# Kernel optimization log

Hardware: AMD Instinct MI355X
Metric: run time of the kernel (lower is better)

## Reference

```python
import jax, jax.numpy as jnp
import numpy as np
from jax import lax

N = 2048        # nodes
F_IN = 512      # input features
D_MODEL = 256
D_INNER = 256   # must equal d_model (shapes in original forward)
DT_RANK = 16
N_STATE = 16    # block ssm state size
LAYER_NUM = 8   # GCN propagation depth == ssm seq len
NUM_CLASSES = 40
HDIM = 8; NHEADS = D_MODEL // HDIM; D_ST2 = 8; D_CONV = 4   # Mamba2 branch
CONV_DIM = D_INNER + 2 * D_ST2
ALPHA = 0.1; GW = 0.5
BN_EPS = 1e-5; RMS_EPS = 1e-5

def setup_inputs():
    key = jax.random.key(0)
    ks = jax.random.split(key, 16)
    def uni(k, shape, s):
        return jax.random.uniform(k, shape, minval=-s, maxval=s, dtype=jnp.float32)
    d_in_proj = 2 * D_INNER + 2 * D_ST2 + NHEADS
    blk_A = jnp.tile(jnp.arange(1, N_STATE + 1, dtype=jnp.float32)[None, :], (D_INNER, 1))
    return {
        "x": jax.random.normal(ks[0], (N, F_IN), dtype=jnp.float32),
        "adj": jax.random.normal(ks[1], (N, N), dtype=jnp.float32) * (0.5 / np.sqrt(N)),
        "lin1_W": uni(ks[2], (F_IN, D_MODEL), 1.0 / np.sqrt(D_MODEL)),
        "m2_in_proj": uni(ks[3], (D_MODEL, d_in_proj), 1.0 / np.sqrt(D_MODEL)),
        "m2_conv_w": uni(ks[4], (CONV_DIM, D_CONV), 1.0 / np.sqrt(D_CONV)),
        "m2_conv_b": jnp.zeros((CONV_DIM,), jnp.float32),
        "m2_dt_bias": uni(ks[5], (NHEADS,), 0.1),
        "m2_A_log": jnp.log(jnp.arange(1, NHEADS + 1, dtype=jnp.float32)),
        "m2_D": jnp.ones((NHEADS,), jnp.float32),
        "m2_norm_w": jnp.ones((D_INNER,), jnp.float32),
        "m2_out_proj": uni(ks[6], (D_INNER, D_MODEL), 1.0 / np.sqrt(D_MODEL)),
        "blk_xproj_W": uni(ks[7], (D_INNER, DT_RANK + 2 * N_STATE), 1.0 / np.sqrt(DT_RANK + 2 * N_STATE)),
        "blk_dtproj_W": uni(ks[8], (DT_RANK, D_INNER), 1.0 / np.sqrt(D_INNER)),
        "blk_A_log": jnp.log(blk_A),
        "blk_D": jnp.ones((D_INNER,), jnp.float32),
        "blk_outproj_W": uni(ks[9], (D_INNER, D_MODEL), 1.0 / np.sqrt(D_MODEL)),
        "bn1_g": jnp.ones((D_MODEL,), jnp.float32),
        "bn1_b": jnp.zeros((D_MODEL,), jnp.float32),
        "bn2_g": jnp.ones((D_MODEL,), jnp.float32),
        "bn2_b": jnp.zeros((D_MODEL,), jnp.float32),
        "lin2_W": uni(ks[10], (D_MODEL, NUM_CLASSES), 1.0 / np.sqrt(NUM_CLASSES)),
    }

def _bn_eval(x, g, b):
    # eval-mode BatchNorm1d with fresh running stats (mean=0, var=1)
    return x * (g / np.sqrt(1.0 + BN_EPS)) + b

def _mamba2(u, in_proj, conv_w, conv_b, dt_bias, A_log, Dp, norm_w, out_proj):
    # u: (b, l, d_model). Mamba2 with expand=1, ngroups=1, headdim=8, d_state=8.
    b, l, _ = u.shape
    zxbcdt = u @ in_proj
    z = zxbcdt[..., :D_INNER]
    xBC = zxbcdt[..., D_INNER:D_INNER + CONV_DIM]
    dt = jax.nn.softplus(zxbcdt[..., -NHEADS:] + dt_bias)          # (b,l,h)
    # causal depthwise conv over sequence
    conv = lax.conv_general_dilated(
        xBC.transpose(0, 2, 1), conv_w[:, None, :], (1,), [(D_CONV - 1, 0)],
        feature_group_count=CONV_DIM)
    xBC = jax.nn.silu(conv.transpose(0, 2, 1) + conv_b)
    xh = xBC[..., :D_INNER].reshape(b, l, NHEADS, HDIM)
    Bm = xBC[..., D_INNER:D_INNER + D_ST2]                          # (b,l,n)
    Cm = xBC[..., D_INNER + D_ST2:]                                 # (b,l,n)
    A = -jnp.exp(A_log)                                             # (h,)
    dA = jnp.exp(dt * A)                                            # (b,l,h)
    dBx = jnp.einsum('blh,bln,blhp->blhpn', dt, Bm, xh)
    def step(s, inp):
        dA_t, dBx_t, C_t = inp
        s = dA_t[:, :, None, None] * s + dBx_t                      # (b,h,p,n)
        return s, jnp.einsum('bhpn,bn->bhp', s, C_t)
    s0 = jnp.zeros((b, NHEADS, HDIM, D_ST2), u.dtype)
    _, ys = lax.scan(step, s0, (dA.transpose(1, 0, 2),
                                dBx.transpose(1, 0, 2, 3, 4),
                                Cm.transpose(1, 0, 2)))
    y = ys.transpose(1, 0, 2, 3) + xh * Dp[None, None, :, None]
    y = y.reshape(b, l, D_INNER)
    g = y * jax.nn.silu(z)                                          # gated RMSNorm
    g = g * lax.rsqrt(jnp.mean(g * g, -1, keepdims=True) + RMS_EPS) * norm_w
    return g @ out_proj

def _gcn_mamba_block(xb, adj, xproj_W, dtproj_W, A_log, Dp, outproj_W):
    # GCN propagation builds the 'sequence' over layers; Mamba selective scan over it.
    feats = [xb]
    xi = xb
    for _ in range(LAYER_NUM - 1):
        xi = adj @ xi
        xi = 0.95 * xi + 0.05 * xb     # alpha=0.05 hardcoded in original forward
        feats.append(xi)
    xs = jnp.stack(feats, axis=1)                                   # (N, L, d)
    x_dbl = jax.nn.relu(xs @ xproj_W)
    delta = jax.nn.softplus(x_dbl[..., :DT_RANK] @ dtproj_W)        # (N,L,d)
    Bm = x_dbl[..., DT_RANK:DT_RANK + N_STATE]
    Cm = x_dbl[..., DT_RANK + N_STATE:]
    A = -jnp.exp(A_log)                                             # (d,n)
    dA = jnp.exp(jnp.einsum('bld,dn->bldn', delta, A))
    dBu = jnp.einsum('bld,bln,bld->bldn', delta, Bm, xs)
    def step(s, inp):
        dA_t, dBu_t, C_t = inp
        s = dA_t * s + dBu_t                                        # (N,d,n)
        return s, jnp.einsum('bdn,bn->bd', s, C_t)
    s0 = jnp.zeros((xs.shape[0], D_INNER, N_STATE), xs.dtype)
    _, ys = lax.scan(step, s0, (dA.transpose(1, 0, 2, 3),
                                dBu.transpose(1, 0, 2, 3),
                                Cm.transpose(1, 0, 2)))
    y = ys.transpose(1, 0, 2) + xs * Dp
    return y @ outproj_W                                            # (N,L,d_model)

def reference(x, adj, lin1_W, m2_in_proj, m2_conv_w, m2_conv_b, m2_dt_bias,
              m2_A_log, m2_D, m2_norm_w, m2_out_proj, blk_xproj_W, blk_dtproj_W,
              blk_A_log, blk_D, blk_outproj_W, bn1_g, bn1_b, bn2_g, bn2_b, lin2_W):
    x_input = x @ lin1_W                                            # (N,d)
    g_in = x_input[None]                                            # (1,N,d)
    m2 = lambda t: _mamba2(t, m2_in_proj, m2_conv_w, m2_conv_b, m2_dt_bias,
                           m2_A_log, m2_D, m2_norm_w, m2_out_proj)
    g_out = m2(g_in) + jnp.flip(m2(jnp.flip(g_in, 1)), 1)
    g_out = jax.nn.relu(g_out)[0] * (1.0 - ALPHA) + ALPHA * x_input
    xb = jax.nn.relu(_bn_eval(x_input, bn1_g, bn1_b))
    all_out = _gcn_mamba_block(xb, adj, blk_xproj_W, blk_dtproj_W,
                               blk_A_log, blk_D, blk_outproj_W)
    output = (all_out[:, -1, :] + x_input) * GW + g_out * (1.0 - GW)
    output = jax.nn.relu(_bn_eval(output, bn2_g, bn2_b))
    all_out = jax.nn.relu(all_out)
    y = output @ lin2_W
    return (all_out, jax.nn.log_softmax(y, axis=-1))
```

## Files before the change

kernel.cpp:

```cpp
#include <hip/hip_runtime.h>
#include <math.h>


typedef _Float16 half8 __attribute__((ext_vector_type(8)));
typedef _Float16 half4v __attribute__((ext_vector_type(4)));
typedef float f32x4 __attribute__((ext_vector_type(4)));

__device__ __forceinline__ float softplus_fast(float x) {
    return fmaxf(x, 0.f) + __logf(1.f + __expf(-fabsf(x)));
}
__device__ __forceinline__ float silu_fast(float x) {
    return __fdividef(x, 1.f + __expf(-x));
}

template<int EPI>
__global__ __launch_bounds__(256) void mm16(
    const _Float16* __restrict__ A16, int lda,
    const _Float16* __restrict__ BT16, int ldb,
    float* __restrict__ dst, _Float16* __restrict__ dst16,
    const _Float16* __restrict__ aux16, _Float16* __restrict__ aux2_16,
    int N, int ldc, int kchunk)
{
    __shared__ _Float16 As[128][40];
    __shared__ _Float16 Bs[64][40];
    const int tid = threadIdx.x;
    const int col0 = blockIdx.x * 64;
    const int row0 = blockIdx.y * 128;
    const int kz = blockIdx.z;
    const int k0 = kz * kchunk;
    const int wave = tid >> 6, lane = tid & 63;
    f32x4 acc[2][4];
    #pragma unroll
    for (int i = 0; i < 2; ++i)
        #pragma unroll
        for (int j = 0; j < 4; ++j)
            acc[i][j] = (f32x4){0.f, 0.f, 0.f, 0.f};
    const int ar = tid >> 1, ac = (tid & 1) * 16;
    const int br = tid >> 2, bc = (tid & 3) * 8;
    const int lrow = lane & 15, kof = (lane >> 4) * 8;
    for (int ks = 0; ks < kchunk; ks += 32) {
        {
            const _Float16* src = A16 + (size_t)(row0 + ar) * lda + k0 + ks + ac;
            *reinterpret_cast<float4*>(&As[ar][ac])     = *reinterpret_cast<const float4*>(src);
            *reinterpret_cast<float4*>(&As[ar][ac + 8]) = *reinterpret_cast<const float4*>(src + 8);
        }
        {
            const _Float16* src = BT16 + (size_t)(col0 + br) * ldb + k0 + ks + bc;
            *reinterpret_cast<float4*>(&Bs[br][bc]) = *reinterpret_cast<const float4*>(src);
        }
        __syncthreads();
        half8 a[2], b[4];
        #pragma unroll
        for (int fr = 0; fr < 2; ++fr)
            a[fr] = *reinterpret_cast<const half8*>(&As[wave * 32 + fr * 16 + lrow][kof]);
        #pragma unroll
        for (int fc = 0; fc < 4; ++fc)
            b[fc] = *reinterpret_cast<const half8*>(&Bs[fc * 16 + lrow][kof]);
        #pragma unroll
        for (int fr = 0; fr < 2; ++fr)
            #pragma unroll
            for (int fc = 0; fc < 4; ++fc)
                acc[fr][fc] = __builtin_amdgcn_mfma_f32_16x16x32_f16(a[fr], b[fc], acc[fr][fc], 0, 0, 0);
        __syncthreads();
    }
    const int col = lane & 15, rbase = (lane >> 4) * 4;
    #pragma unroll
    for (int fr = 0; fr < 2; ++fr)
        #pragma unroll
        for (int fc = 0; fc < 4; ++fc) {
            int c = col0 + fc * 16 + col;
            #pragma unroll
            for (int i = 0; i < 4; ++i) {
                int m = row0 + wave * 32 + fr * 16 + rbase + i;
                float v = acc[fr][fc][i];
                if (EPI == 0) {
                    _Float16* P = dst16 + (size_t)kz * gridDim.y * 128 * 256;
                    P[(size_t)m * 256 + c] = (_Float16)v;
                } else if (EPI == 1) {
                    if (c < N) dst[(size_t)m * ldc + c] = fmaxf(v, 0.f);
                } else if (EPI == 2) {
                    dst16[(size_t)m * 256 + c] =
                        (_Float16)(fmaxf(v, 0.f) * 0.9f + 0.1f * (float)aux16[(size_t)m * 256 + c]);
                } else if (EPI == 3) {
                    int bb = m & 2047, ll = m >> 11;
                    dst[(size_t)((bb << 3) + ll) * 256 + c] = fmaxf(v, 0.f);
                    if (ll == 7) aux2_16[(size_t)bb * 256 + c] = (_Float16)v;
                } else if (EPI == 4) {
                    dst16[(size_t)m * 256 + c] = (_Float16)v;
                } else {
                    if (c < N) dst16[(size_t)m * ldc + c] = (_Float16)v;
                }
            }
        }
}

__global__ __launch_bounds__(256) void k_combine16(
    const _Float16* __restrict__ psum16, const _Float16* __restrict__ xb16,
    _Float16* __restrict__ xi16, _Float16* __restrict__ fT16)
{
    int m0 = (blockIdx.x >> 3) * 32, n0 = (blockIdx.x & 7) * 32;
    int row = threadIdx.x >> 3;
    int c4  = (threadIdx.x & 7) * 4;
    __shared__ float T[32][33];
    size_t idx = (size_t)(m0 + row) * 256 + n0 + c4;
    float s[4] = {0.f, 0.f, 0.f, 0.f};
    #pragma unroll
    for (int q = 0; q < 4; ++q) {
        half4v pv = *reinterpret_cast<const half4v*>(&psum16[idx + (size_t)q * 524288]);
        s[0] += (float)pv[0]; s[1] += (float)pv[1];
        s[2] += (float)pv[2]; s[3] += (float)pv[3];
    }
    half4v xv = *reinterpret_cast<const half4v*>(&xb16[idx]);
    half4v ov;
    #pragma unroll
    for (int j = 0; j < 4; ++j) {
        float v = 0.95f * s[j] + 0.05f * (float)xv[j];
        ov[j] = (_Float16)v;
        T[row][c4 + j] = v;
    }
    *reinterpret_cast<half4v*>(&xi16[idx]) = ov;
    __syncthreads();
    int tx = threadIdx.x & 31, tg = threadIdx.x >> 5;
    #pragma unroll
    for (int j = 0; j < 4; ++j) {
        int n = tg * 4 + j;
        fT16[(size_t)(n0 + n) * 2048 + m0 + tx] = (_Float16)T[tx][n];
    }
}

__global__ __launch_bounds__(256) void k_prep(
    const float* __restrict__ x, const float* __restrict__ adj,
    const float* __restrict__ lin1W, const float* __restrict__ inproj,
    const float* __restrict__ outprj, const float* __restrict__ xprojW,
    const float* __restrict__ boutW,
    _Float16* __restrict__ x16, _Float16* __restrict__ adj16,
    _Float16* __restrict__ lin1WT, _Float16* __restrict__ inprojT,
    _Float16* __restrict__ outprjT, _Float16* __restrict__ xprojT,
    _Float16* __restrict__ WT16)
{
    int b = blockIdx.x, tid = threadIdx.x;
    if (b < 5120) {
        const float* src = (b < 1024) ? x : adj;
        _Float16* o = (b < 1024) ? x16 : adj16;
        int lb = (b < 1024) ? b : b - 1024;
        int i = (lb * 256 + tid) * 4;
        float4 v = *reinterpret_cast<const float4*>(&src[i]);
        half4v h;
        h[0] = (_Float16)v.x; h[1] = (_Float16)v.y; h[2] = (_Float16)v.z; h[3] = (_Float16)v.w;
        *reinterpret_cast<half4v*>(&o[i]) = h;
    } else if (b < 5632) {
        int idx = (b - 5120) * 256 + tid;
        int n = idx >> 9, k = idx & 511;
        lin1WT[idx] = (_Float16)lin1W[(size_t)k * 256 + n];
    } else if (b < 6208) {
        int idx = (b - 5632) * 256 + tid;
        int n = idx >> 8, k = idx & 255;
        inprojT[idx] = (n < 560) ? (_Float16)inproj[(size_t)k * 560 + n] : (_Float16)0.f;
    } else if (b < 6464) {
        int idx = (b - 6208) * 256 + tid;
        int n = idx >> 8, k = idx & 255;
        outprjT[idx] = (_Float16)outprj[(size_t)k * 256 + n];
    } else if (b < 6528) {
        int idx = (b - 6464) * 256 + tid;
        int n = idx >> 8, k = idx & 255;
        xprojT[idx] = (n < 48) ? (_Float16)xprojW[(size_t)k * 48 + n] : (_Float16)0.f;
    } else {
        int idx = (b - 6528) * 256 + tid;
        int n = idx >> 8, k = idx & 255;
        WT16[idx] = (_Float16)boutW[(size_t)k * 256 + n];
    }
}

__global__ __launch_bounds__(256) void k_xb_t16(
    const _Float16* __restrict__ X16, const float* __restrict__ g, const float* __restrict__ b,
    _Float16* __restrict__ f16a, _Float16* __restrict__ fT16)
{
    const float sc = 0.99999500003749951f;
    int m0 = (blockIdx.x >> 3) * 32, n0 = (blockIdx.x & 7) * 32;
    int tx = threadIdx.x & 31, tg = threadIdx.x >> 5;
    __shared__ float T[32][33];
    float gd = g[n0 + tx] * sc, bd = b[n0 + tx];
    #pragma unroll
    for (int i = 0; i < 4; ++i) {
        int m = tg * 4 + i;
        size_t idx = (size_t)(m0 + m) * 256 + n0 + tx;
        float v = fmaxf((float)X16[idx] * gd + bd, 0.f);
        f16a[idx] = (_Float16)v;
        T[m][tx] = v;
    }
    __syncthreads();
    #pragma unroll
    for (int j = 0; j < 4; ++j) {
        int n = tg * 4 + j;
        fT16[(size_t)(n0 + n) * 2048 + m0 + tx] = (_Float16)T[tx][n];
    }
}

__global__ __launch_bounds__(320) void k_conv(
    const _Float16* __restrict__ Z16, const float* __restrict__ w, const float* __restrict__ bconv,
    float* __restrict__ xhf, float* __restrict__ Bf, float* __restrict__ Cf,
    float* __restrict__ xhr, float* __restrict__ Br, float* __restrict__ Cr)
{
    int bx = blockIdx.x;
    int dir = bx >> 11, t = bx & 2047;
    int c = threadIdx.x;
    if (c >= 272) return;
    float acc = bconv[c];
    #pragma unroll
    for (int k = 0; k < 4; ++k) {
        int tt = dir ? (t + 3 - k) : (t - 3 + k);
        if (tt >= 0 && tt < 2048) acc = fmaf(w[c * 4 + k], (float)Z16[(size_t)tt * 560 + 256 + c], acc);
    }
    float v = silu_fast(acc);
    float* xh = dir ? xhr : xhf;
    float* B  = dir ? Br  : Bf;
    float* C  = dir ? Cr  : Cf;
    if (c < 256)       xh[(size_t)t * 256 + c] = v;
    else if (c < 264)  B[(size_t)t * 8 + (c - 256)] = v;
    else               C[(size_t)t * 8 + (c - 264)] = v;
}

__global__ __launch_bounds__(64) void k_scan_m2_p1(
    const _Float16* __restrict__ Z16, const float* __restrict__ dtbias, const float* __restrict__ A_log,
    const float* __restrict__ xhf, const float* __restrict__ Bf, const float* __restrict__ Cf,
    const float* __restrict__ xhr, const float* __restrict__ Br, const float* __restrict__ Cr,
    const float* __restrict__ Dvec,
    float* __restrict__ yf, float* __restrict__ yr,
    float* __restrict__ Ptbuf,
    float* __restrict__ Acbuf,
    float* __restrict__ Sloc)
{
    int bid = blockIdx.x;
    int c  = bid & 31;
    int hh = bid >> 5;
    int dir = hh >> 5, h = hh & 31;
    const float* xhp = dir ? xhr : xhf;
    const float* Bp  = dir ? Br  : Bf;
    const float* Cp  = dir ? Cr  : Cf;
    float* yp        = dir ? yr  : yf;
    int lane = threadIdx.x;
    int p = lane >> 3, n = lane & 7;
    float Dh = Dvec[h];
    __shared__ float dts[64];
    __shared__ float dAs[64];
    __shared__ float Ps[64][8];
    __shared__ float Bs[64][8];
    __shared__ float Cs[64][8];
    __shared__ float Ys[64][8];
    __shared__ float Pts[64];
    const int j0 = c * 64;
    {
        int j = j0 + lane;
        int t = dir ? (2047 - j) : j;
        float v = (float)Z16[(size_t)t * 560 + 528 + h] + dtbias[h];
        float dtv = softplus_fast(v);
        dts[lane] = dtv;
        dAs[lane] = __expf(-dtv * __expf(A_log[h]));
    }
    __syncthreads();
    #pragma unroll
    for (int q = 0; q < 8; ++q) {
        int idx = q * 64 + lane;
        int i = idx >> 3, e = idx & 7;
        int j = j0 + i;
        int t = dir ? (2047 - j) : j;
        Ps[i][e] = dts[i] * xhp[(size_t)t * 256 + h * 8 + e];
        Bs[i][e] = Bp[(size_t)t * 8 + e];
        Cs[i][e] = Cp[(size_t)t * 8 + e];
    }
    __syncthreads();
    float s = 0.f;
    float P = 1.f;
    for (int i = 0; i < 64; ++i) {
        float a = dAs[i];
        float u = Ps[i][p] * Bs[i][n];
        s = fmaf(a, s, u);
        P *= a;
        float yv = s * Cs[i][n];
        yv += __shfl_xor(yv, 1);
        yv += __shfl_xor(yv, 2);
        yv += __shfl_xor(yv, 4);
        if (n == 0) Ys[i][p] = yv;
        if (lane == 0) Pts[i] = P;
    }
    __syncthreads();
    #pragma unroll
    for (int q = 0; q < 8; ++q) {
        int idx = q * 64 + lane;
        int i = idx >> 3, e = idx & 7;
        int j = j0 + i;
        int t = dir ? (2047 - j) : j;
        yp[(size_t)t * 256 + h * 8 + e] = Ys[i][e] + xhp[(size_t)t * 256 + h * 8 + e] * Dh;
    }
    {
        int j = j0 + lane;
        Ptbuf[((size_t)dir * 2048 + j) * 32 + h] = Pts[lane];
    }
    if (lane == 0) Acbuf[hh * 32 + c] = P;
    Sloc[((size_t)hh * 32 + c) * 64 + lane] = s;
}

__global__ __launch_bounds__(64) void k_scan_m2_p2(
    const float* __restrict__ Acbuf, const float* __restrict__ Sloc,
    float* __restrict__ Sstart)
{
    int hh = blockIdx.x;
    int lane = threadIdx.x;
    float s = 0.f;
    for (int c = 0; c < 32; ++c) {
        Sstart[((size_t)hh * 32 + c) * 64 + lane] = s;
        float a = Acbuf[hh * 32 + c];
        s = fmaf(a, s, Sloc[((size_t)hh * 32 + c) * 64 + lane]);
    }
}

__global__ __launch_bounds__(256) void k_gate(
    const _Float16* __restrict__ Z16, const float* __restrict__ yf, const float* __restrict__ yr,
    const float* __restrict__ Cf, const float* __restrict__ Cr,
    const float* __restrict__ Ptbuf, const float* __restrict__ Sstart,
    const float* __restrict__ nw, _Float16* __restrict__ gsum16)
{
    int t = blockIdx.x, d = threadIdx.x;
    int h = d >> 3, p = d & 7;
    __shared__ float Csh[2][8];
    if (d < 8)       Csh[0][d] = Cf[(size_t)t * 8 + d];
    else if (d < 16) Csh[1][d - 8] = Cr[(size_t)t * 8 + (d - 8)];
    __syncthreads();
    int jf = t, jr = 2047 - t;
    int cf = jf >> 6, cr = jr >> 6;
    float Ptf = Ptbuf[((size_t)jf) * 32 + h];
    float Ptr = Ptbuf[((size_t)2048 + jr) * 32 + h];
    const float* ssf = &Sstart[(((size_t)h) * 32 + cf) * 64 + p * 8];
    const float* ssr = &Sstart[(((size_t)(32 + h)) * 32 + cr) * 64 + p * 8];
    float dotf = 0.f, dotr = 0.f;
    #pragma unroll
    for (int n2 = 0; n2 < 8; ++n2) {
        dotf = fmaf(ssf[n2], Csh[0][n2], dotf);
        dotr = fmaf(ssr[n2], Csh[1][n2], dotr);
    }
    float yfv = yf[(size_t)t * 256 + d] + Ptf * dotf;
    float yrv = yr[(size_t)t * 256 + d] + Ptr * dotr;
    float zv = (float)Z16[(size_t)t * 560 + d];
    float sz = silu_fast(zv);
    float gf = yfv * sz;
    float gr = yrv * sz;
    float vf = gf * gf, vr = gr * gr;
    for (int o = 32; o > 0; o >>= 1) { vf += __shfl_down(vf, o); vr += __shfl_down(vr, o); }
    __shared__ float sfa[4], sra[4];
    __shared__ float tot[2];
    int wid = d >> 6;
    if ((d & 63) == 0) { sfa[wid] = vf; sra[wid] = vr; }
    __syncthreads();
    if (d == 0) {
        tot[0] = sfa[0] + sfa[1] + sfa[2] + sfa[3];
        tot[1] = sra[0] + sra[1] + sra[2] + sra[3];
    }
    __syncthreads();
    float inf_ = rsqrtf(tot[0] / 256.f + 1e-5f);
    float inr_ = rsqrtf(tot[1] / 256.f + 1e-5f);
    gsum16[(size_t)t * 256 + d] = (_Float16)((gf * inf_ + gr * inr_) * nw[d]);
}

__global__ __launch_bounds__(256) void k_scan_gcn(
    const float* __restrict__ xdbl,
    const float* __restrict__ dtW,
    const float* __restrict__ A_log,
    const float* __restrict__ Dv,
    _Float16* __restrict__ f16io)
{
    int b = blockIdx.x, d = threadIdx.x;
    __shared__ float xrow[8][48];
    for (int j = d; j < 384; j += 256) {
        int l = j / 48, k = j % 48;
        xrow[l][k] = xdbl[(size_t)(l * 2048 + b) * 48 + k];
    }
    __syncthreads();
    float a[16];
    #pragma unroll
    for (int n = 0; n < 16; ++n) a[n] = -__expf(A_log[d * 16 + n]);
    float Dd = Dv[d];
    float s[16];
    #pragma unroll
    for (int n = 0; n < 16; ++n) s[n] = 0.f;
    for (int l = 0; l < 8; ++l) {
        float accd = 0.f;
        #pragma unroll
        for (int k = 0; k < 16; ++k) accd = fmaf(xrow[l][k], dtW[k * 256 + d], accd);
        float dl = softplus_fast(accd);
        size_t r = (size_t)(l * 2048 + b) * 256 + d;
        float xv = (float)f16io[r];
        float du = dl * xv;
        float y = 0.f;
        #pragma unroll
        for (int n = 0; n < 16; ++n) {
            float dAn = __expf(dl * a[n]);
            s[n] = fmaf(dAn, s[n], du * xrow[l][16 + n]);
            y = fmaf(s[n], xrow[l][32 + n], y);
        }
        f16io[r] = (_Float16)(y + xv * Dd);
    }
}

__global__ __launch_bounds__(256) void k_head(
    const _Float16* __restrict__ lastl16, const _Float16* __restrict__ X16,
    const _Float16* __restrict__ gout16,
    const float* __restrict__ g2, const float* __restrict__ b2, const float* __restrict__ W2,
    float* __restrict__ out1)
{
    int b = blockIdx.x, d = threadIdx.x;
    __shared__ float ov[256];
    __shared__ float yv[40];
    const float sc = 0.99999500003749951f;
    float v = ((float)lastl16[(size_t)b * 256 + d] + (float)X16[(size_t)b * 256 + d]) * 0.5f
              + (float)gout16[(size_t)b * 256 + d] * 0.5f;
    v = v * (g2[d] * sc) + b2[d];
    ov[d] = fmaxf(v, 0.f);
    __syncthreads();
    if (d < 40) {
        float acc = 0.f;
        for (int k = 0; k < 256; ++k) acc = fmaf(ov[k], W2[k * 40 + d], acc);
        yv[d] = acc;
    }
    __syncthreads();
    if (d < 40) {
        float m = -1e30f;
        for (int j = 0; j < 40; ++j) m = fmaxf(m, yv[j]);
        float se = 0.f;
        for (int j = 0; j < 40; ++j) se += expf(yv[j] - m);
        out1[(size_t)b * 40 + d] = yv[d] - m - logf(se);
    }
}

extern "C" void kernel_launch(void* const* d_in, const int* in_sizes, int n_in,
                              void* d_out, int out_size, void* d_ws, size_t ws_size,
                              hipStream_t stream)
{
    const float* x      = (const float*)d_in[0];
    const float* adj    = (const float*)d_in[1];
    const float* lin1W  = (const float*)d_in[2];
    const float* inproj = (const float*)d_in[3];
    const float* convw  = (const float*)d_in[4];
    const float* convb  = (const float*)d_in[5];
    const float* dtbias = (const float*)d_in[6];
    const float* m2Alog = (const float*)d_in[7];
    const float* m2D    = (const float*)d_in[8];
    const float* normw  = (const float*)d_in[9];
    const float* outprj = (const float*)d_in[10];
    const float* xprojW = (const float*)d_in[11];
    const float* dtprjW = (const float*)d_in[12];
    const float* bAlog  = (const float*)d_in[13];
    const float* bD     = (const float*)d_in[14];
    const float* boutW  = (const float*)d_in[15];
    const float* bn1g   = (const float*)d_in[16];
    const float* bn1b   = (const float*)d_in[17];
    const float* bn2g   = (const float*)d_in[18];
    const float* bn2b   = (const float*)d_in[19];
    const float* lin2W  = (const float*)d_in[20];
    float* out = (float*)d_out;
    float* ws  = (float*)d_ws;

    float* xhf   = ws + 1802240;
    float* Bf    = ws + 2326528;
    float* Cf    = ws + 2342912;
    float* xhr   = ws + 2359296;
    float* Br    = ws + 2883584;
    float* Cr    = ws + 2899968;
    float* yf    = ws + 2916352;
    float* yr    = ws + 3440640;
    float* xdbl  = ws + 9207808;
    float* scr    = ws + 10518528;
    float* Ptbuf  = scr;
    float* Acbuf  = scr + 131072;
    float* Sloc   = scr + 133120;
    float* Sstart = scr + 264192;
    _Float16* psum16 = (_Float16*)(ws + 10518528);
    _Float16* Z16       = (_Float16*)(ws + 524288);
    _Float16* gout16    = (_Float16*)(ws + 4489216);
    _Float16* lastl16   = (_Float16*)(ws + 9994240);
    _Float16* adj16h    = (_Float16*)(ws + 14712832);
    _Float16* fT16A     = (_Float16*)(ws + 16809984);
    _Float16* WT16h     = (_Float16*)(ws + 17072128);
    _Float16* x16       = (_Float16*)(ws + 17104896);
    _Float16* lin1WT16  = (_Float16*)(ws + 17629184);
    _Float16* inprojT16 = (_Float16*)(ws + 17694720);
    _Float16* outprjT16 = (_Float16*)(ws + 17768448);
    _Float16* xprojT16  = (_Float16*)(ws + 17801216);
    _Float16* X16       = (_Float16*)(ws + 17809408);
    _Float16* gsum16    = (_Float16*)(ws + 18071552);
    _Float16* feats16a  = (_Float16*)(ws + 18333696);
    (void)ws_size; (void)in_sizes; (void)n_in; (void)out_size;

    dim3 blk(256);
    k_prep<<<dim3(6784), blk, 0, stream>>>(x, adj, lin1W, inproj, outprj, xprojW, boutW,
                                           x16, adj16h, lin1WT16, inprojT16, outprjT16,
                                           xprojT16, WT16h);
    mm16<4><<<dim3(4, 16, 1), blk, 0, stream>>>(x16, 512, lin1WT16, 512, nullptr, X16, nullptr, nullptr, 256, 256, 512);
    mm16<5><<<dim3(9, 16, 1), blk, 0, stream>>>(X16, 256, inprojT16, 256, nullptr, Z16, nullptr, nullptr, 560, 560, 256);
    k_conv<<<dim3(4096), dim3(320), 0, stream>>>(Z16, convw, convb, xhf, Bf, Cf, xhr, Br, Cr);
    k_scan_m2_p1<<<dim3(2048), dim3(64), 0, stream>>>(Z16, dtbias, m2Alog, xhf, Bf, Cf, xhr, Br, Cr,
                                                      m2D, yf, yr, Ptbuf, Acbuf, Sloc);
    k_scan_m2_p2<<<dim3(64), dim3(64), 0, stream>>>(Acbuf, Sloc, Sstart);
    k_gate<<<dim3(2048), blk, 0, stream>>>(Z16, yf, yr, Cf, Cr, Ptbuf, Sstart, normw, gsum16);
    mm16<2><<<dim3(4, 16, 1), blk, 0, stream>>>(gsum16, 256, outprjT16, 256, nullptr, gout16, X16, nullptr, 256, 256, 256);
    k_xb_t16<<<dim3(512), blk, 0, stream>>>(X16, bn1g, bn1b, feats16a, fT16A);
    for (int i = 1; i < 8; ++i) {
        mm16<0><<<dim3(4, 16, 4), blk, 0, stream>>>(adj16h, 2048, fT16A, 2048, nullptr, psum16, nullptr, nullptr, 256, 256, 512);
        k_combine16<<<dim3(512), blk, 0, stream>>>(psum16, feats16a,
                                                   feats16a + (size_t)i * 524288, fT16A);
    }
    mm16<1><<<dim3(1, 128, 1), blk, 0, stream>>>(feats16a, 256, xprojT16, 256, xdbl, nullptr, nullptr, nullptr, 48, 48, 256);
    k_scan_gcn<<<dim3(2048), blk, 0, stream>>>(xdbl, dtprjW, bAlog, bD, feats16a);
    mm16<3><<<dim3(4, 128, 1), blk, 0, stream>>>(feats16a, 256, WT16h, 256, out, nullptr, nullptr, lastl16, 256, 256, 256);
    k_head<<<dim3(2048), blk, 0, stream>>>(lastl16, X16, gout16, bn2g, bn2b, lin2W, out + 4194304);
}
```

Before: 240.1 us.

## Fuse depthwise conv into scan/gate kernels and double split-K for adjacency matmul

Removes the separate k_conv kernel and its fp32 intermediate buffers (xh, B, C for both directions); the conv+SiLU is recomputed on the fly inside the scan kernel and the gate kernel, which now read Z16 directly. The per-layer adjacency GEMM goes from 4 to 8 split-K chunks of 256, and the combine kernel sums 8 partials, raising block count for the small 2048x256 output. Tradeoffs: redundant conv work (B/C recomputed per head block), more partial-sum traffic, and the loops are no longer unrolled.

Result: no change. 243.9 us (+1.6%).

```diff
diff --git a/kernel.cpp b/kernel.cpp
--- a/kernel.cpp
+++ b/kernel.cpp
@@ -11,6 +11,19 @@
 }
 __device__ __forceinline__ float silu_fast(float x) {
     return __fdividef(x, 1.f + __expf(-x));
+}
+__device__ __forceinline__ float conv_silu(
+    const _Float16* __restrict__ Z16, const float* __restrict__ w,
+    const float* __restrict__ b, int ch, int t, int dir)
+{
+    float acc = b[ch];
+    #pragma unroll
+    for (int k = 0; k < 4; ++k) {
+        int tt = dir ? (t + 3 - k) : (t - 3 + k);
+        if (tt >= 0 && tt < 2048)
+            acc = fmaf(w[ch * 4 + k], (float)Z16[(size_t)tt * 560 + 256 + ch], acc);
+    }
+    return silu_fast(acc);
 }
 
 template<int EPI>
@@ -105,7 +118,7 @@
     size_t idx = (size_t)(m0 + row) * 256 + n0 + c4;
     float s[4] = {0.f, 0.f, 0.f, 0.f};
     #pragma unroll
-    for (int q = 0; q < 4; ++q) {
+    for (int q = 0; q < 8; ++q) {
         half4v pv = *reinterpret_cast<const half4v*>(&psum16[idx + (size_t)q * 524288]);
         s[0] += (float)pv[0]; s[1] += (float)pv[1];
         s[2] += (float)pv[2]; s[3] += (float)pv[3];
@@ -196,34 +209,9 @@
     }
 }
 
-__global__ __launch_bounds__(320) void k_conv(
-    const _Float16* __restrict__ Z16, const float* __restrict__ w, const float* __restrict__ bconv,
-    float* __restrict__ xhf, float* __restrict__ Bf, float* __restrict__ Cf,
-    float* __restrict__ xhr, float* __restrict__ Br, float* __restrict__ Cr)
-{
-    int bx = blockIdx.x;
-    int dir = bx >> 11, t = bx & 2047;
-    int c = threadIdx.x;
-    if (c >= 272) return;
-    float acc = bconv[c];
-    #pragma unroll
-    for (int k = 0; k < 4; ++k) {
-        int tt = dir ? (t + 3 - k) : (t - 3 + k);
-        if (tt >= 0 && tt < 2048) acc = fmaf(w[c * 4 + k], (float)Z16[(size_t)tt * 560 + 256 + c], acc);
-    }
-    float v = silu_fast(acc);
-    float* xh = dir ? xhr : xhf;
-    float* B  = dir ? Br  : Bf;
-    float* C  = dir ? Cr  : Cf;
-    if (c < 256)       xh[(size_t)t * 256 + c] = v;
-    else if (c < 264)  B[(size_t)t * 8 + (c - 256)] = v;
-    else               C[(size_t)t * 8 + (c - 264)] = v;
-}
-
 __global__ __launch_bounds__(64) void k_scan_m2_p1(
     const _Float16* __restrict__ Z16, const float* __restrict__ dtbias, const float* __restrict__ A_log,
-    const float* __restrict__ xhf, const float* __restrict__ Bf, const float* __restrict__ Cf,
-    const float* __restrict__ xhr, const float* __restrict__ Br, const float* __restrict__ Cr,
+    const float* __restrict__ convw, const float* __restrict__ convb,
     const float* __restrict__ Dvec,
     float* __restrict__ yf, float* __restrict__ yr,
     float* __restrict__ Ptbuf,
@@ -234,15 +222,13 @@
     int c  = bid & 31;
     int hh = bid >> 5;
     int dir = hh >> 5, h = hh & 31;
-    const float* xhp = dir ? xhr : xhf;
-    const float* Bp  = dir ? Br  : Bf;
-    const float* Cp  = dir ? Cr  : Cf;
-    float* yp        = dir ? yr  : yf;
+    float* yp = dir ? yr : yf;
     int lane = threadIdx.x;
     int p = lane >> 3, n = lane & 7;
     float Dh = Dvec[h];
     __shared__ float dts[64];
     __shared__ float dAs[64];
+    __shared__ float xhs[64][8];
     __shared__ float Ps[64][8];
     __shared__ float Bs[64][8];
     __shared__ float Cs[64][8];
@@ -258,15 +244,16 @@
         dAs[lane] = __expf(-dtv * __expf(A_log[h]));
     }
     __syncthreads();
-    #pragma unroll
     for (int q = 0; q < 8; ++q) {
         int idx = q * 64 + lane;
         int i = idx >> 3, e = idx & 7;
         int j = j0 + i;
         int t = dir ? (2047 - j) : j;
-        Ps[i][e] = dts[i] * xhp[(size_t)t * 256 + h * 8 + e];
-        Bs[i][e] = Bp[(size_t)t * 8 + e];
-        Cs[i][e] = Cp[(size_t)t * 8 + e];
+        float xh = conv_silu(Z16, convw, convb, h * 8 + e, t, dir);
+        xhs[i][e] = xh;
+        Ps[i][e] = dts[i] * xh;
+        Bs[i][e] = conv_silu(Z16, convw, convb, 256 + e, t, dir);
+        Cs[i][e] = conv_silu(Z16, convw, convb, 264 + e, t, dir);
     }
     __syncthreads();
     float s = 0.f;
@@ -284,13 +271,12 @@
         if (lane == 0) Pts[i] = P;
     }
     __syncthreads();
-    #pragma unroll
     for (int q = 0; q < 8; ++q) {
         int idx = q * 64 + lane;
         int i = idx >> 3, e = idx & 7;
         int j = j0 + i;
         int t = dir ? (2047 - j) : j;
-        yp[(size_t)t * 256 + h * 8 + e] = Ys[i][e] + xhp[(size_t)t * 256 + h * 8 + e] * Dh;
+        yp[(size_t)t * 256 + h * 8 + e] = Ys[i][e] + xhs[i][e] * Dh;
     }
     {
         int j = j0 + lane;
@@ -316,15 +302,15 @@
 
 __global__ __launch_bounds__(256) void k_gate(
     const _Float16* __restrict__ Z16, const float* __restrict__ yf, const float* __restrict__ yr,
-    const float* __restrict__ Cf, const float* __restrict__ Cr,
+    const float* __restrict__ convw, const float* __restrict__ convb,
     const float* __restrict__ Ptbuf, const float* __restrict__ Sstart,
     const float* __restrict__ nw, _Float16* __restrict__ gsum16)
 {
     int t = blockIdx.x, d = threadIdx.x;
     int h = d >> 3, p = d & 7;
     __shared__ float Csh[2][8];
-    if (d < 8)       Csh[0][d] = Cf[(size_t)t * 8 + d];
-    else if (d < 16) Csh[1][d - 8] = Cr[(size_t)t * 8 + (d - 8)];
+    if (d < 8)       Csh[0][d] = conv_silu(Z16, convw, convb, 264 + d, t, 0);
+    else if (d < 16) Csh[1][d - 8] = conv_silu(Z16, convw, convb, 264 + (d - 8), t, 1);
     __syncthreads();
     int jf = t, jr = 2047 - t;
     int cf = jf >> 6, cr = jr >> 6;
@@ -459,12 +445,6 @@
     float* out = (float*)d_out;
     float* ws  = (float*)d_ws;
 
-    float* xhf   = ws + 1802240;
-    float* Bf    = ws + 2326528;
-    float* Cf    = ws + 2342912;
-    float* xhr   = ws + 2359296;
-    float* Br    = ws + 2883584;
-    float* Cr    = ws + 2899968;
     float* yf    = ws + 2916352;
     float* yr    = ws + 3440640;
     float* xdbl  = ws + 9207808;
@@ -496,15 +476,14 @@
                                            xprojT16, WT16h);
     mm16<4><<<dim3(4, 16, 1), blk, 0, stream>>>(x16, 512, lin1WT16, 512, nullptr, X16, nullptr, nullptr, 256, 256, 512);
     mm16<5><<<dim3(9, 16, 1), blk, 0, stream>>>(X16, 256, inprojT16, 256, nullptr, Z16, nullptr, nullptr, 560, 560, 256);
-    k_conv<<<dim3(4096), dim3(320), 0, stream>>>(Z16, convw, convb, xhf, Bf, Cf, xhr, Br, Cr);
-    k_scan_m2_p1<<<dim3(2048), dim3(64), 0, stream>>>(Z16, dtbias, m2Alog, xhf, Bf, Cf, xhr, Br, Cr,
+    k_scan_m2_p1<<<dim3(2048), dim3(64), 0, stream>>>(Z16, dtbias, m2Alog, convw, convb,
                                                       m2D, yf, yr, Ptbuf, Acbuf, Sloc);
     k_scan_m2_p2<<<dim3(64), dim3(64), 0, stream>>>(Acbuf, Sloc, Sstart);
-    k_gate<<<dim3(2048), blk, 0, stream>>>(Z16, yf, yr, Cf, Cr, Ptbuf, Sstart, normw, gsum16);
+    k_gate<<<dim3(2048), blk, 0, stream>>>(Z16, yf, yr, convw, convb, Ptbuf, Sstart, normw, gsum16);
     mm16<2><<<dim3(4, 16, 1), blk, 0, stream>>>(gsum16, 256, outprjT16, 256, nullptr, gout16, X16, nullptr, 256, 256, 256);
     k_xb_t16<<<dim3(512), blk, 0, stream>>>(X16, bn1g, bn1b, feats16a, fT16A);
     for (int i = 1; i < 8; ++i) {
-        mm16<0><<<dim3(4, 16, 4), blk, 0, stream>>>(adj16h, 2048, fT16A, 2048, nullptr, psum16, nullptr, nullptr, 256, 256, 512);
+        mm16<0><<<dim3(4, 16, 8), blk, 0, stream>>>(adj16h, 2048, fT16A, 2048, nullptr, psum16, nullptr, nullptr, 256, 256, 256);
         k_combine16<<<dim3(512), blk, 0, stream>>>(psum16, feats16a,
                                                    feats16a + (size_t)i * 524288, fT16A);
     }
```
